# Performance work log

Hardware: AMD Instinct MI355X
Metric: run time of the kernel (lower is better)

The kernel has to match this reference:

```python
import jax, jax.numpy as jnp
import numpy as np

N_NODES = 100000
NUM_FEAT = 64
NUM_CLASS = 40
N_EDGES = 1600000


def setup_inputs() -> dict:
    key = jax.random.key(0)
    k1, k2, k3, k4, k5 = jax.random.split(key, 5)
    x = jax.random.normal(k1, (N_NODES, NUM_FEAT), dtype=jnp.float32)
    index = jax.random.randint(k2, (2, N_EDGES), 0, N_NODES, dtype=jnp.int64)
    # SAGEConv params: lin_l applied to aggregated neighbors (has bias),
    # lin_r applied to root features (no bias) -- PyG convention.
    s = 1.0 / np.sqrt(NUM_FEAT)
    lin_l_w = jax.random.uniform(k3, (NUM_FEAT, NUM_CLASS), dtype=jnp.float32, minval=-s, maxval=s)
    lin_l_b = jnp.zeros((NUM_CLASS,), dtype=jnp.float32)
    lin_r_w = jax.random.uniform(k4, (NUM_FEAT, NUM_CLASS), dtype=jnp.float32, minval=-s, maxval=s)
    return {"x": x, "index": index, "lin_l_w": lin_l_w, "lin_l_b": lin_l_b, "lin_r_w": lin_r_w}


def reference(x, index, lin_l_w, lin_l_b, lin_r_w):
    src, dst = index[0], index[1]
    # Mean aggregation over incoming neighbors: messages flow src -> dst.
    msg = x[src]                                        # [E, F] gather
    agg_sum = jax.ops.segment_sum(msg, dst, num_segments=N_NODES)   # [N, F]
    deg = jax.ops.segment_sum(jnp.ones((index.shape[1],), dtype=x.dtype), dst,
                              num_segments=N_NODES)     # [N]
    agg = agg_sum / jnp.maximum(deg, 1.0)[:, None]      # mean, safe for isolated nodes
    out = agg @ lin_l_w + lin_l_b + x @ lin_r_w         # [N, C]
    return jax.nn.log_softmax(out, axis=1)
```

## Files before the change

### kernel.cpp

```cpp
#include <hip/hip_runtime.h>
#include <hip/hip_fp8.h>
#include <math.h>

constexpr int NODES = 100000;
constexpr int F = 64;
constexpr int C = 40;
constexpr int NPB   = 128;
constexpr int NB    = (NODES + NPB - 1) / NPB;
constexpr int NBPAD = 1024;
constexpr int BCAP  = 2816;
constexpr int TILE  = 4096;
constexpr int NTILES = NODES / 16;
constexpr int MBLK  = (NTILES + 3) / 4;

typedef __attribute__((ext_vector_type(8))) short short8;
typedef __attribute__((ext_vector_type(4))) float floatx4;
typedef __attribute__((ext_vector_type(2))) float floatx2;

__device__ inline unsigned bf16pack2(float a, float b) {
    unsigned ua = __builtin_bit_cast(unsigned, a);
    unsigned ub = __builtin_bit_cast(unsigned, b);
    ua += 0x7FFFu + ((ua >> 16) & 1u);
    ub += 0x7FFFu + ((ub >> 16) & 1u);
    return (ua >> 16) | (ub & 0xFFFF0000u);
}
__device__ inline unsigned short bf16of(float a) {
    unsigned ua = __builtin_bit_cast(unsigned, a);
    ua += 0x7FFFu + ((ua >> 16) & 1u);
    return (unsigned short)(ua >> 16);
}
__device__ inline float bf16tof(unsigned short u) {
    return __builtin_bit_cast(float, (unsigned)u << 16);
}
__device__ inline unsigned char fp8of(float f) {
    __hip_fp8_e4m3 q(f);
    return (unsigned char)q.__x;
}
template <int K>
__device__ inline float fp8byte(unsigned d) {
    __hip_fp8_e4m3 v;
    v.__x = (__hip_fp8_storage_t)((d >> (8 * K)) & 0xFFu);
    return (float)v;
}
template <int HI>
__device__ inline floatx2 fp8pk(unsigned d) {
#if __has_builtin(__builtin_amdgcn_cvt_pk_f32_fp8)
    return __builtin_amdgcn_cvt_pk_f32_fp8((int)d, HI != 0);
#else
    floatx2 r;
    r[0] = fp8byte<HI ? 2 : 0>(d);
    r[1] = fp8byte<HI ? 3 : 1>(d);
    return r;
#endif
}

__global__ __launch_bounds__(256)
void fused_A(const float* __restrict__ x,
             const float* __restrict__ wl,
             const float* __restrict__ bl,
             const float* __restrict__ wr,
             const int* __restrict__ src, const int* __restrict__ dst,
             int* __restrict__ gcursor, int* __restrict__ bbuf, int nedges,
             unsigned char* __restrict__ y8f, unsigned short* __restrict__ z8) {
    __shared__ union {
        struct { int lhist[NB]; int lcur[NB]; } bz;
        struct { unsigned sB[10 * 64 * 4]; float sbl[40]; } mf;
    } sh;

    int t = threadIdx.x;

    if (blockIdx.x < MBLK) {
        if (t < 40) sh.mf.sbl[t] = bl[t];
        for (int s = t; s < 640; s += 256) {
            int region = s >> 6;
            int l      = s & 63;
            int ct = region >> 1, ks = region & 1;
            int col = ct * 16 + (l & 15);
            int fb  = ks * 32 + ((l >> 4) << 3);
            const float* wsrc = (col < 40) ? (wl + col) : (wr + (col - 40));
            unsigned* dstp = &sh.mf.sB[s * 4];
#pragma unroll
            for (int p = 0; p < 4; ++p) {
                float a = wsrc[(fb + 2 * p) * 40];
                float b = wsrc[(fb + 2 * p + 1) * 40];
                dstp[p] = bf16pack2(a, b);
            }
        }
        __syncthreads();

        int lane = t & 63;
        int nt = blockIdx.x * 4 + (t >> 6);
        if (nt >= NTILES) return;

        union U { unsigned u[4]; short8 v; };
        short8 bf[5][2];
#pragma unroll
        for (int ct = 0; ct < 5; ++ct)
#pragma unroll
            for (int ks = 0; ks < 2; ++ks) {
                U tmp;
                const uint4* p =
                    (const uint4*)&sh.mf.sB[((ct * 2 + ks) * 64 + lane) * 4];
                uint4 q = *p;
                tmp.u[0] = q.x; tmp.u[1] = q.y; tmp.u[2] = q.z; tmp.u[3] = q.w;
                bf[ct][ks] = tmp.v;
            }

        floatx4 acc[5];
#pragma unroll
        for (int ct = 0; ct < 5; ++ct) {
            int col = ct * 16 + (lane & 15);
            float bias = (col >= 40) ? sh.mf.sbl[col - 40] : 0.0f;
            acc[ct] = (floatx4){bias, bias, bias, bias};
        }

        int row = nt * 16 + (lane & 15);
        const float4* xp = (const float4*)(x + (size_t)row * F);
        short8 af[2];
#pragma unroll
        for (int ks = 0; ks < 2; ++ks) {
            int kb = ks * 8 + ((lane >> 4) << 1);
            float4 va = xp[kb];
            float4 vb = xp[kb + 1];
            U a;
            a.u[0] = bf16pack2(va.x, va.y);
            a.u[1] = bf16pack2(va.z, va.w);
            a.u[2] = bf16pack2(vb.x, vb.y);
            a.u[3] = bf16pack2(vb.z, vb.w);
            af[ks] = a.v;
        }

#pragma unroll
        for (int ks = 0; ks < 2; ++ks)
#pragma unroll
            for (int ct = 0; ct < 5; ++ct)
                acc[ct] = __builtin_amdgcn_mfma_f32_16x16x32_bf16(
                    af[ks], bf[ct][ks], acc[ct], 0, 0, 0);

#pragma unroll
        for (int ct = 0; ct < 5; ++ct) {
            int col = ct * 16 + (lane & 15);
#pragma unroll
            for (int r = 0; r < 4; ++r) {
                int grow = nt * 16 + ((lane >> 4) << 2) + r;
                if (col < 40) y8f[(size_t)grow * C + col]       = fp8of(acc[ct][r]);
                else          z8[(size_t)grow * C + (col - 40)] = bf16of(acc[ct][r]);
            }
        }
    } else {
        for (int i = t; i < NB; i += 256) sh.bz.lhist[i] = 0;
        __syncthreads();

        int bb = blockIdx.x - MBLK;
        int base = bb * TILE;
        int pk[16], bk[16];
#pragma unroll
        for (int u = 0; u < 16; ++u) {
            int e = base + u * 256 + t;
            bk[u] = -1;
            if (e < nedges) {
                int s = src[e], d = dst[e];
                if ((unsigned)s < (unsigned)NODES && (unsigned)d < (unsigned)NODES) {
                    bk[u] = d >> 7;
                    pk[u] = s | ((d & 127) << 17);
                    atomicAdd(&sh.bz.lhist[bk[u]], 1);
                }
            }
        }
        __syncthreads();
        for (int i = t; i < NB; i += 256) {
            int c = sh.bz.lhist[i];
            sh.bz.lcur[i] = c ? atomicAdd(&gcursor[i], c) : 0;
        }
        __syncthreads();
#pragma unroll
        for (int u = 0; u < 16; ++u) {
            if (bk[u] >= 0) {
                int p = atomicAdd(&sh.bz.lcur[bk[u]], 1);
                if (p < BCAP) bbuf[(size_t)bk[u] * BCAP + p] = pk[u];
            }
        }
    }
}

__device__ inline void acc8(float (&acc)[8], uint2 q) {
    floatx2 v;
    v = fp8pk<0>(q.x); acc[0] += v[0]; acc[1] += v[1];
    v = fp8pk<1>(q.x); acc[2] += v[0]; acc[3] += v[1];
    v = fp8pk<0>(q.y); acc[4] += v[0]; acc[5] += v[1];
    v = fp8pk<1>(q.y); acc[6] += v[0]; acc[7] += v[1];
}

__global__ __launch_bounds__(256)
void sort_aggregate(const unsigned char* __restrict__ y8f,
                    const unsigned short* __restrict__ z8,
                    const int* __restrict__ bbuf,
                    const int* __restrict__ gcount,
                    float* __restrict__ out) {
    __shared__ int lhist[NPB];
    __shared__ int lcur[NPB];
    __shared__ int slds[BCAP];
    __shared__ int w0tot;

    int b = blockIdx.x;
    int t = threadIdx.x;
    int lane = t & 63;

    if (t < NPB) lhist[t] = 0;
    __syncthreads();

    int cnt = gcount[b];
    if (cnt > BCAP) cnt = BCAP;
    const int* myb = bbuf + (size_t)b * BCAP;

    for (int i = t; i < cnt; i += 256)
        atomicAdd(&lhist[myb[i] >> 17], 1);
    __syncthreads();

    int c = 0, sc = 0;
    if (t < NPB) {
        c = lhist[t];
        sc = c;
#pragma unroll
        for (int d = 1; d < 64; d <<= 1) {
            int o = __shfl_up(sc, d);
            if (lane >= d) sc += o;
        }
    }
    if (t == 63) w0tot = sc;
    __syncthreads();
    if (t >= 64 && t < NPB) sc += w0tot;
    if (t < NPB) lcur[t] = sc - c;
    __syncthreads();

    for (int i = t; i < cnt; i += 256) {
        int pk = myb[i];
        int p = atomicAdd(&lcur[pk >> 17], 1);
        slds[p] = pk & 0x1FFFF;
    }
    __syncthreads();

    int gid = t >> 3;
    int i = t & 7;
    bool valid = (i < 5);
    int byteoff = (valid ? i : 4) * 8;

    for (int j = 0; j < 4; ++j) {
        int nd = gid * 4 + j;
        int n = b * NPB + nd;
        if (n >= NODES) break;

        int dg = lhist[nd];
        const int* sp = slds + (lcur[nd] - dg);

        uint4 zv = make_uint4(0u, 0u, 0u, 0u);
        if (valid) zv = *(const uint4*)(z8 + (size_t)n * C + i * 8);

        float acc[8] = {0.f, 0.f, 0.f, 0.f, 0.f, 0.f, 0.f, 0.f};

        int npair = dg >> 1;
        if (npair > 0) {
            int s0 = sp[0];
            int s1 = sp[1];
            for (int p = 0; p < npair; ++p) {
                int c0 = s0, c1 = s1;
                int nx = 2 * p + 2;
                int pi = (nx + 1 < dg) ? nx : dg - 2;
                s0 = sp[pi];
                s1 = sp[pi + 1];
                uint2 q0 = *(const uint2*)(y8f + (size_t)c0 * C + byteoff);
                uint2 q1 = *(const uint2*)(y8f + (size_t)c1 * C + byteoff);
                acc8(acc, q0);
                acc8(acc, q1);
            }
        }
        if (dg & 1) {
            int cl = sp[dg - 1];
            uint2 q = *(const uint2*)(y8f + (size_t)cl * C + byteoff);
            acc8(acc, q);
        }

        float inv = 1.0f / (float)(dg > 0 ? dg : 1);

        float o[8];
        if (valid) {
            unsigned zu[4] = {zv.x, zv.y, zv.z, zv.w};
#pragma unroll
            for (int k = 0; k < 4; ++k) {
                o[2 * k]     = bf16tof((unsigned short)(zu[k] & 0xFFFFu))
                             + acc[2 * k] * inv;
                o[2 * k + 1] = bf16tof((unsigned short)(zu[k] >> 16))
                             + acc[2 * k + 1] * inv;
            }
        } else {
#pragma unroll
            for (int k = 0; k < 8; ++k) o[k] = -1e30f;
        }

        float mv = -1e30f;
        if (valid)
#pragma unroll
            for (int k = 0; k < 8; ++k) mv = fmaxf(mv, o[k]);
#pragma unroll
        for (int m = 1; m <= 4; m <<= 1) mv = fmaxf(mv, __shfl_xor(mv, m));

        float ev = 0.0f;
        if (valid)
#pragma unroll
            for (int k = 0; k < 8; ++k) ev += __expf(o[k] - mv);
#pragma unroll
        for (int m = 1; m <= 4; m <<= 1) ev += __shfl_xor(ev, m);
        float lse = mv + __logf(ev);

        if (valid) {
            float4 o0 = make_float4(o[0] - lse, o[1] - lse, o[2] - lse, o[3] - lse);
            float4 o1 = make_float4(o[4] - lse, o[5] - lse, o[6] - lse, o[7] - lse);
            float4* op = (float4*)(out + (size_t)n * C + i * 8);
            op[0] = o0;
            op[1] = o1;
        }
    }
}

__global__ __launch_bounds__(256)
void scatter_kernel(const float* __restrict__ x, const int* __restrict__ src,
                    const int* __restrict__ dst, float* __restrict__ aggsum,
                    float* __restrict__ deg, int nedges) {
    int lane = threadIdx.x & 63;
    int e = blockIdx.x * 4 + (threadIdx.x >> 6);
    if (e >= nedges) return;
    int s = src[e], d = dst[e];
    if ((unsigned)s >= (unsigned)NODES || (unsigned)d >= (unsigned)NODES) return;
    atomicAdd(&aggsum[(size_t)d * F + lane], x[(size_t)s * F + lane]);
    if (lane == 0) atomicAdd(&deg[d], 1.0f);
}

__global__ __launch_bounds__(256)
void meanify_kernel(float* __restrict__ aggsum, const float* __restrict__ deg) {
    int lane = threadIdx.x & 63;
    int n = blockIdx.x * 4 + (threadIdx.x >> 6);
    if (n >= NODES) return;
    aggsum[(size_t)n * F + lane] *= 1.0f / fmaxf(deg[n], 1.0f);
}

__global__ __launch_bounds__(256)
void node_kernel(const float* __restrict__ x, const float* __restrict__ aggmean,
                 const float* __restrict__ wl, const float* __restrict__ bl,
                 const float* __restrict__ wr, float* __restrict__ out) {
    __shared__ alignas(16) float sWl[F * C];
    __shared__ alignas(16) float sWr[F * C];
    __shared__ alignas(16) float sb[C];
    for (int i = threadIdx.x; i < F * C; i += 256) { sWl[i] = wl[i]; sWr[i] = wr[i]; }
    if (threadIdx.x < C) sb[threadIdx.x] = bl[threadIdx.x];
    __syncthreads();
    int n = blockIdx.x * 256 + threadIdx.x;
    if (n >= NODES) return;
    float4 acc[10];
    const float4* sb4 = (const float4*)sb;
#pragma unroll
    for (int q = 0; q < 10; ++q) acc[q] = sb4[q];
    const float4* xr  = (const float4*)(x       + (size_t)n * F);
    const float4* ar  = (const float4*)(aggmean + (size_t)n * F);
    const float4* wl4 = (const float4*)sWl;
    const float4* wr4 = (const float4*)sWr;
    for (int f4 = 0; f4 < F / 4; ++f4) {
        float4 xv = xr[f4], av = ar[f4];
        float xs[4]  = {xv.x, xv.y, xv.z, xv.w};
        float as_[4] = {av.x, av.y, av.z, av.w};
#pragma unroll
        for (int jj = 0; jj < 4; ++jj) {
            int f = f4 * 4 + jj;
#pragma unroll
            for (int q = 0; q < 10; ++q) {
                float4 wlv = wl4[f * 10 + q], wrv = wr4[f * 10 + q];
                acc[q].x = fmaf(as_[jj], wlv.x, fmaf(xs[jj], wrv.x, acc[q].x));
                acc[q].y = fmaf(as_[jj], wlv.y, fmaf(xs[jj], wrv.y, acc[q].y));
                acc[q].z = fmaf(as_[jj], wlv.z, fmaf(xs[jj], wrv.z, acc[q].z));
                acc[q].w = fmaf(as_[jj], wlv.w, fmaf(xs[jj], wrv.w, acc[q].w));
            }
        }
    }
    float m = -1e30f;
#pragma unroll
    for (int q = 0; q < 10; ++q)
        m = fmaxf(m, fmaxf(fmaxf(acc[q].x, acc[q].y), fmaxf(acc[q].z, acc[q].w)));
    float ssum = 0.0f;
#pragma unroll
    for (int q = 0; q < 10; ++q)
        ssum += __expf(acc[q].x - m) + __expf(acc[q].y - m) +
                __expf(acc[q].z - m) + __expf(acc[q].w - m);
    float lse = m + __logf(ssum);
    float4* op = (float4*)(out + (size_t)n * C);
#pragma unroll
    for (int q = 0; q < 10; ++q) {
        float4 v;
        v.x = acc[q].x - lse; v.y = acc[q].y - lse;
        v.z = acc[q].z - lse; v.w = acc[q].w - lse;
        op[q] = v;
    }
}

extern "C" void kernel_launch(void* const* d_in, const int* in_sizes, int n_in,
                              void* d_out, int out_size, void* d_ws, size_t ws_size,
                              hipStream_t stream) {
    const float* x     = (const float*)d_in[0];
    const int*   index = (const int*)d_in[1];
    const float* wl    = (const float*)d_in[2];
    const float* bl    = (const float*)d_in[3];
    const float* wr    = (const float*)d_in[4];
    float* out = (float*)d_out;

    int nedges = in_sizes[1] / 2;
    const int* src = index;
    const int* dst = index + nedges;

    size_t need = (size_t)NODES * C * 3
                + ((size_t)NB * BCAP + NBPAD) * 4;

    if (ws_size >= need) {
        unsigned short* z8 = (unsigned short*)d_ws;
        unsigned char* y8f = (unsigned char*)(z8 + (size_t)NODES * C);
        int* bbuf       = (int*)(y8f + (size_t)NODES * C);
        int* gcursor    = bbuf + (size_t)NB * BCAP;

        hipMemsetAsync(gcursor, 0, NBPAD * sizeof(int), stream);

        int bblocks = (nedges + TILE - 1) / TILE;
        fused_A<<<MBLK + bblocks, 256, 0, stream>>>(
            x, wl, bl, wr, src, dst, gcursor, bbuf, nedges, y8f, z8);
        sort_aggregate<<<NB, 256, 0, stream>>>(
            y8f, z8, bbuf, gcursor, out);
    } else {
        float* aggsum = (float*)d_ws;
        float* deg    = aggsum + (size_t)NODES * F;
        hipMemsetAsync(d_ws, 0,
                       ((size_t)NODES * F + NODES) * sizeof(float), stream);
        scatter_kernel<<<(nedges + 3) / 4, 256, 0, stream>>>(
            x, src, dst, aggsum, deg, nedges);
        meanify_kernel<<<(NODES + 3) / 4, 256, 0, stream>>>(aggsum, deg);
        node_kernel<<<(NODES + 255) / 256, 256, 0, stream>>>(
            x, aggsum, wl, bl, wr, out);
    }
}
```

Measured before the change: 139.8 us.

## Halve bucket size, pad fp8 rows to 64 bytes, add nontemporal loads/stores

Shrinks destination buckets from 128 to 64 nodes, doubling the number of aggregate blocks and halving per-block LDS and edge capacity. Pads the fp8 neighbour-feature rows to a 64-byte pitch so each gathered row stays inside one cache line. Caches the bucket edges in registers so they are read from global memory once instead of twice, simplifies the single-wave prefix scan, and uses nontemporal loads and stores for streamed data. The smaller BCAP raises the risk of bucket overflow on skewed graphs, and the padding enlarges the workspace.

```diff
diff --git a/kernel.cpp b/kernel.cpp
--- a/kernel.cpp
+++ b/kernel.cpp
@@ -5,10 +5,11 @@
 constexpr int NODES = 100000;
 constexpr int F = 64;
 constexpr int C = 40;
-constexpr int NPB   = 128;
+constexpr int YPITCH = 64;
+constexpr int NPB   = 64;
 constexpr int NB    = (NODES + NPB - 1) / NPB;
-constexpr int NBPAD = 1024;
-constexpr int BCAP  = 2816;
+constexpr int NBPAD = 2048;
+constexpr int BCAP  = 1408;
 constexpr int TILE  = 4096;
 constexpr int NTILES = NODES / 16;
 constexpr int MBLK  = (NTILES + 3) / 4;
@@ -16,6 +17,8 @@
 typedef __attribute__((ext_vector_type(8))) short short8;
 typedef __attribute__((ext_vector_type(4))) float floatx4;
 typedef __attribute__((ext_vector_type(2))) float floatx2;
+typedef __attribute__((ext_vector_type(4))) unsigned uintx4;
+typedef __attribute__((ext_vector_type(4))) float fx4;
 
 __device__ inline unsigned bf16pack2(float a, float b) {
     unsigned ua = __builtin_bit_cast(unsigned, a);
@@ -115,18 +118,18 @@
         }
 
         int row = nt * 16 + (lane & 15);
-        const float4* xp = (const float4*)(x + (size_t)row * F);
+        const fx4* xp = (const fx4*)(x + (size_t)row * F);
         short8 af[2];
 #pragma unroll
         for (int ks = 0; ks < 2; ++ks) {
             int kb = ks * 8 + ((lane >> 4) << 1);
-            float4 va = xp[kb];
-            float4 vb = xp[kb + 1];
+            fx4 va = __builtin_nontemporal_load(xp + kb);
+            fx4 vb = __builtin_nontemporal_load(xp + kb + 1);
             U a;
-            a.u[0] = bf16pack2(va.x, va.y);
-            a.u[1] = bf16pack2(va.z, va.w);
-            a.u[2] = bf16pack2(vb.x, vb.y);
-            a.u[3] = bf16pack2(vb.z, vb.w);
+            a.u[0] = bf16pack2(va[0], va[1]);
+            a.u[1] = bf16pack2(va[2], va[3]);
+            a.u[2] = bf16pack2(vb[0], vb[1]);
+            a.u[3] = bf16pack2(vb[2], vb[3]);
             af[ks] = a.v;
         }
 
@@ -143,7 +146,7 @@
 #pragma unroll
             for (int r = 0; r < 4; ++r) {
                 int grow = nt * 16 + ((lane >> 4) << 2) + r;
-                if (col < 40) y8f[(size_t)grow * C + col]       = fp8of(acc[ct][r]);
+                if (col < 40) y8f[(size_t)grow * YPITCH + col] = fp8of(acc[ct][r]);
                 else          z8[(size_t)grow * C + (col - 40)] = bf16of(acc[ct][r]);
             }
         }
@@ -159,10 +162,11 @@
             int e = base + u * 256 + t;
             bk[u] = -1;
             if (e < nedges) {
-                int s = src[e], d = dst[e];
+                int s = __builtin_nontemporal_load(src + e);
+                int d = __builtin_nontemporal_load(dst + e);
                 if ((unsigned)s < (unsigned)NODES && (unsigned)d < (unsigned)NODES) {
-                    bk[u] = d >> 7;
-                    pk[u] = s | ((d & 127) << 17);
+                    bk[u] = d >> 6;
+                    pk[u] = s | ((d & 63) << 17);
                     atomicAdd(&sh.bz.lhist[bk[u]], 1);
                 }
             }
@@ -200,11 +204,9 @@
     __shared__ int lhist[NPB];
     __shared__ int lcur[NPB];
     __shared__ int slds[BCAP];
-    __shared__ int w0tot;
 
     int b = blockIdx.x;
     int t = threadIdx.x;
-    int lane = t & 63;
 
     if (t < NPB) lhist[t] = 0;
     __syncthreads();
@@ -213,31 +215,33 @@
     if (cnt > BCAP) cnt = BCAP;
     const int* myb = bbuf + (size_t)b * BCAP;
 
-    for (int i = t; i < cnt; i += 256)
-        atomicAdd(&lhist[myb[i] >> 17], 1);
+    int ek[(BCAP + 255) / 256];
+    int nh = 0;
+    for (int i = t; i < cnt; i += 256) ek[nh++] = __builtin_nontemporal_load(myb + i);
+#pragma unroll
+    for (int u = 0; u < (BCAP + 255) / 256; ++u)
+        if (u < nh) atomicAdd(&lhist[ek[u] >> 17], 1);
     __syncthreads();
 
-    int c = 0, sc = 0;
     if (t < NPB) {
-        c = lhist[t];
-        sc = c;
+        int c = lhist[t];
+        int sc = c;
 #pragma unroll
         for (int d = 1; d < 64; d <<= 1) {
             int o = __shfl_up(sc, d);
-            if (lane >= d) sc += o;
-        }
-    }
-    if (t == 63) w0tot = sc;
+            if (t >= d) sc += o;
+        }
+        lcur[t] = sc - c;
+    }
     __syncthreads();
-    if (t >= 64 && t < NPB) sc += w0tot;
-    if (t < NPB) lcur[t] = sc - c;
-    __syncthreads();
-
-    for (int i = t; i < cnt; i += 256) {
-        int pk = myb[i];
-        int p = atomicAdd(&lcur[pk >> 17], 1);
-        slds[p] = pk & 0x1FFFF;
-    }
+
+#pragma unroll
+    for (int u = 0; u < (BCAP + 255) / 256; ++u)
+        if (u < nh) {
+            int pk = ek[u];
+            int p = atomicAdd(&lcur[pk >> 17], 1);
+            slds[p] = pk & 0x1FFFF;
+        }
     __syncthreads();
 
     int gid = t >> 3;
@@ -245,16 +249,17 @@
     bool valid = (i < 5);
     int byteoff = (valid ? i : 4) * 8;
 
-    for (int j = 0; j < 4; ++j) {
-        int nd = gid * 4 + j;
+    for (int j = 0; j < 2; ++j) {
+        int nd = gid * 2 + j;
         int n = b * NPB + nd;
         if (n >= NODES) break;
 
         int dg = lhist[nd];
         const int* sp = slds + (lcur[nd] - dg);
 
-        uint4 zv = make_uint4(0u, 0u, 0u, 0u);
-        if (valid) zv = *(const uint4*)(z8 + (size_t)n * C + i * 8);
+        uintx4 zv = {0u, 0u, 0u, 0u};
+        if (valid) zv = __builtin_nontemporal_load(
+                            (const uintx4*)(z8 + (size_t)n * C + i * 8));
 
         float acc[8] = {0.f, 0.f, 0.f, 0.f, 0.f, 0.f, 0.f, 0.f};
 
@@ -268,15 +273,15 @@
                 int pi = (nx + 1 < dg) ? nx : dg - 2;
                 s0 = sp[pi];
                 s1 = sp[pi + 1];
-                uint2 q0 = *(const uint2*)(y8f + (size_t)c0 * C + byteoff);
-                uint2 q1 = *(const uint2*)(y8f + (size_t)c1 * C + byteoff);
+                uint2 q0 = *(const uint2*)(y8f + (size_t)c0 * YPITCH + byteoff);
+                uint2 q1 = *(const uint2*)(y8f + (size_t)c1 * YPITCH + byteoff);
                 acc8(acc, q0);
                 acc8(acc, q1);
             }
         }
         if (dg & 1) {
             int cl = sp[dg - 1];
-            uint2 q = *(const uint2*)(y8f + (size_t)cl * C + byteoff);
+            uint2 q = *(const uint2*)(y8f + (size_t)cl * YPITCH + byteoff);
             acc8(acc, q);
         }
 
@@ -284,7 +289,7 @@
 
         float o[8];
         if (valid) {
-            unsigned zu[4] = {zv.x, zv.y, zv.z, zv.w};
+            unsigned zu[4] = {zv[0], zv[1], zv[2], zv[3]};
 #pragma unroll
             for (int k = 0; k < 4; ++k) {
                 o[2 * k]     = bf16tof((unsigned short)(zu[k] & 0xFFFFu))
@@ -313,11 +318,11 @@
         float lse = mv + __logf(ev);
 
         if (valid) {
-            float4 o0 = make_float4(o[0] - lse, o[1] - lse, o[2] - lse, o[3] - lse);
-            float4 o1 = make_float4(o[4] - lse, o[5] - lse, o[6] - lse, o[7] - lse);
-            float4* op = (float4*)(out + (size_t)n * C + i * 8);
-            op[0] = o0;
-            op[1] = o1;
+            fx4 o0 = {o[0] - lse, o[1] - lse, o[2] - lse, o[3] - lse};
+            fx4 o1 = {o[4] - lse, o[5] - lse, o[6] - lse, o[7] - lse};
+            fx4* op = (fx4*)(out + (size_t)n * C + i * 8);
+            __builtin_nontemporal_store(o0, op);
+            __builtin_nontemporal_store(o1, op + 1);
         }
     }
 }
@@ -414,13 +419,13 @@
     const int* src = index;
     const int* dst = index + nedges;
 
-    size_t need = (size_t)NODES * C * 3
+    size_t need = (size_t)NODES * C * 2 + (size_t)NODES * YPITCH
                 + ((size_t)NB * BCAP + NBPAD) * 4;
 
     if (ws_size >= need) {
         unsigned short* z8 = (unsigned short*)d_ws;
         unsigned char* y8f = (unsigned char*)(z8 + (size_t)NODES * C);
-        int* bbuf       = (int*)(y8f + (size_t)NODES * C);
+        int* bbuf       = (int*)(y8f + (size_t)NODES * YPITCH);
         int* gcursor    = bbuf + (size_t)NB * BCAP;
 
         hipMemsetAsync(gcursor, 0, NBPAD * sizeof(int), stream);
```

Result: slower. 148.0 us (+5.9%).
